# Performance work log

Hardware: AMD Instinct MI355X
Metric: run time of the kernel (lower is better)

Reference implementation:

```python
import jax, jax.numpy as jnp
import numpy as np

V_CNT = 10000
B = 16
N = B * V_CNT          # total nodes
K = 6                  # Chebyshev order
CH = [3, 128, 64, 32, 128]
G = 8                  # GroupNorm groups (divides 128, 64, 32)
EPS = 1e-5
AVG_DEG = 16


def setup_inputs() -> dict:
    key = jax.random.key(0)
    ks = jax.random.split(key, 8)
    n_edges = N * AVG_DEG
    inp = {
        "x": jax.random.normal(ks[0], (N, CH[0]), jnp.float32),
        "edge_index": jax.random.randint(ks[1], (2, n_edges), 0, N, jnp.int32).astype(jnp.int64),
    }
    for l in range(3):
        cin, cout = CH[l], CH[l + 1]
        s = (1.0 / (cin * K)) ** 0.5
        inp[f"W{l}"] = jax.random.uniform(ks[2 + l], (K, cin, cout), jnp.float32, -s, s)
        inp[f"b{l}"] = jnp.zeros((cout,), jnp.float32)
        inp[f"gamma{l}"] = jnp.ones((cout,), jnp.float32)
        inp[f"beta{l}"] = jnp.zeros((cout,), jnp.float32)
    din = V_CNT * CH[3]
    s = (1.0 / din) ** 0.5
    inp["W_last"] = jax.random.uniform(ks[5], (din, CH[4]), jnp.float32, -s, s)
    inp["b_last"] = jnp.zeros((CH[4],), jnp.float32)
    return inp


def _cheb_edge_weights(edge_index):
    # PyG ChebConv sym normalization with lambda_max=2: L_hat = L - I = -D^{-1/2} A D^{-1/2}
    row, col = edge_index[0], edge_index[1]
    deg = jax.ops.segment_sum(jnp.ones(row.shape, jnp.float32), row, num_segments=N)
    dis = jnp.where(deg > 0, jax.lax.rsqrt(jnp.maximum(deg, 1.0)), 0.0)  # deg^{-1/2}, inf->0
    return -dis[row] * dis[col], row, col


def _cheb_conv(x, row, col, w, W, b):
    # Chebyshev recursion: Tx0=x, Tx1=L_hat x, Tx_k = 2 L_hat Tx_{k-1} - Tx_{k-2}
    prop = lambda h: jax.ops.segment_sum(w[:, None] * h[col], row, num_segments=N)
    Tx0 = x
    out = Tx0 @ W[0]
    Tx1 = prop(Tx0)
    out = out + Tx1 @ W[1]
    for k in range(2, W.shape[0]):
        Tx2 = 2.0 * prop(Tx1) - Tx0
        out = out + Tx2 @ W[k]
        Tx0, Tx1 = Tx1, Tx2
    return out + b


def _group_norm(h, gamma, beta):
    n, C = h.shape
    hg = h.reshape(n, G, C // G)
    mu = hg.mean(axis=2, keepdims=True)
    var = hg.var(axis=2, keepdims=True)
    hg = (hg - mu) * jax.lax.rsqrt(var + EPS)
    return hg.reshape(n, C) * gamma + beta


def reference(x, edge_index, W0, b0, gamma0, beta0, W1, b1, gamma1, beta1,
              W2, b2, gamma2, beta2, W_last, b_last):
    w, row, col = _cheb_edge_weights(edge_index)
    Ws = [W0, W1, W2]
    bs = [b0, b1, b2]
    gs = [gamma0, gamma1, gamma2]
    betas = [beta0, beta1, beta2]
    h = x
    for l in range(3):
        h = _cheb_conv(h, row, col, w, Ws[l], bs[l])
        h = _group_norm(h, gs[l], betas[l])
        h = jax.nn.relu(h)
    h = h.reshape(-1, V_CNT * CH[3])  # [B, v_cnt*32]
    return h @ W_last + b_last
```

## Files before the change

### kernel.cpp

```cpp
#include <hip/hip_runtime.h>
#include <hip/hip_fp16.h>


#define NN 160000
#define EE 2560000
#define FD2 256
#define NBKT 625
#define BCAPL 13
#define ABLK 500
#define EPT 20

typedef __attribute__((ext_vector_type(8))) _Float16 half8;
typedef __attribute__((ext_vector_type(4))) float floatx4;

__device__ inline float2 h2f2(unsigned u) {
  __half2 h = __builtin_bit_cast(__half2, u);
  return __half22float2(h);
}
__device__ inline unsigned short f2h(float f) {
  return __builtin_bit_cast(unsigned short, __float2half_rn(f));
}
__device__ inline unsigned packh2(float a, float b) {
  return __builtin_bit_cast(unsigned, __floats2half2_rn(a, b));
}

template <int CIN, int COUT>
__device__ inline void combine_item(const float* __restrict__ W, unsigned short* __restrict__ Bt, int idx) {
  int co = idx % COUT;
  int j  = (idx / COUT) % 6;
  int ci = idx / (6 * COUT);
  float c0, c1, c2, c3, c4, c5;
  switch (j) {
    case 0:  c0 = 1;  c1 = 0;  c2 = -1; c3 = 0;   c4 = 1;  c5 = 0;   break;
    case 1:  c0 = 0;  c1 = 1;  c2 = 0;  c3 = -3;  c4 = 0;  c5 = 5;   break;
    case 2:  c0 = 0;  c1 = 0;  c2 = 2;  c3 = 0;   c4 = -8; c5 = 0;   break;
    case 3:  c0 = 0;  c1 = 0;  c2 = 0;  c3 = 4;   c4 = 0;  c5 = -20; break;
    case 4:  c0 = 0;  c1 = 0;  c2 = 0;  c3 = 0;   c4 = 8;  c5 = 0;   break;
    default: c0 = 0;  c1 = 0;  c2 = 0;  c3 = 0;   c4 = 0;  c5 = 16;  break;
  }
  float s = 0.f;
  s += c0 * W[(0 * CIN + ci) * COUT + co];
  s += c1 * W[(1 * CIN + ci) * COUT + co];
  s += c2 * W[(2 * CIN + ci) * COUT + co];
  s += c3 * W[(3 * CIN + ci) * COUT + co];
  s += c4 * W[(4 * CIN + ci) * COUT + co];
  s += c5 * W[(5 * CIN + ci) * COUT + co];
  Bt[(j * COUT + co) * CIN + ci] = f2h(s);
}

__global__ __launch_bounds__(256) void k_prep(const float* __restrict__ W0, const float* __restrict__ W1,
                                              const float* __restrict__ W2, const float* __restrict__ x,
                                              int* __restrict__ bcur, unsigned short* __restrict__ Cwt0,
                                              unsigned short* __restrict__ Cwt1, unsigned short* __restrict__ Cwt2,
                                              float* __restrict__ A3, unsigned short* __restrict__ TxAll) {
  int idx = blockIdx.x * 256 + threadIdx.x;
  if (idx < NBKT) { bcur[idx] = idx << BCAPL; return; }
  idx -= NBKT;
  if (idx < 128 * 32) {
    int co = idx >> 5, t = idx & 31;
    Cwt0[co * 32 + t] = (t < 18) ? f2h(W0[t * 128 + co]) : (unsigned short)0;
    return;
  }
  idx -= 128 * 32;
  if (idx < 128 * 6 * 64) { combine_item<128, 64>(W1, Cwt1, idx); return; }
  idx -= 128 * 6 * 64;
  if (idx < 64 * 6 * 32) { combine_item<64, 32>(W2, Cwt2, idx); return; }
  idx -= 64 * 6 * 32;
  if (idx < NN) {
    int i = idx;
    float v0 = x[i * 3], v1 = x[i * 3 + 1], v2 = x[i * 3 + 2];
    A3[i * 3] = v0; A3[i * 3 + 1] = v1; A3[i * 3 + 2] = v2;
    uint4* dst = reinterpret_cast<uint4*>(TxAll + (size_t)i * 32);
    uint4 z = make_uint4(0u, 0u, 0u, 0u);
    dst[0] = make_uint4(packh2(v0, v1), (unsigned)f2h(v2), 0u, 0u);
    dst[1] = z; dst[2] = z; dst[3] = z;
  }
}

__global__ __launch_bounds__(256) void k_bucketA(const int* __restrict__ ei,
                                                 int* __restrict__ bcur, unsigned* __restrict__ stg) {
  __shared__ int bcnt[NBKT];
  __shared__ int gbase[NBKT];
  int tid = threadIdx.x;
  for (int i = tid; i < NBKT; i += 256) bcnt[i] = 0;
  __syncthreads();
  int r[EPT];
  int e0 = blockIdx.x * (256 * EPT);
#pragma unroll
  for (int k = 0; k < EPT; k++) {
    int e = e0 + k * 256 + tid;
    r[k] = ei[e];
    atomicAdd(&bcnt[r[k] >> 8], 1);
  }
  __syncthreads();
  for (int i = tid; i < NBKT; i += 256) {
    gbase[i] = atomicAdd(&bcur[i], bcnt[i]);
    bcnt[i] = 0;
  }
  __syncthreads();
#pragma unroll
  for (int k = 0; k < EPT; k++) {
    int e = e0 + k * 256 + tid;
    int c = ei[EE + e];
    int b = r[k] >> 8;
    int off = atomicAdd(&bcnt[b], 1);
    int pos = gbase[b] + off;
    if (pos < ((b + 1) << BCAPL))
      stg[pos] = ((unsigned)(r[k] & 255) << 18) | (unsigned)c;
  }
}

__global__ __launch_bounds__(256) void k_bucketB1(const unsigned* __restrict__ stg, const int* __restrict__ bcur,
                                                  int* __restrict__ rowStart, float* __restrict__ dis,
                                                  int* __restrict__ deg) {
  __shared__ int degl[256];
  __shared__ int s[256];
  __shared__ int red[256];
  int b = blockIdx.x;
  int tid = threadIdx.x;
  int part = 0;
  for (int j = tid; j < NBKT; j += 256) {
    int cj = bcur[j] - (j << BCAPL);
    if (cj > (1 << BCAPL)) cj = 1 << BCAPL;
    if (j < b) part += cj;
  }
  red[tid] = part;
  degl[tid] = 0;
  __syncthreads();
  for (int off = 128; off > 0; off >>= 1) {
    if (tid < off) red[tid] += red[tid + off];
    __syncthreads();
  }
  int bbase = red[0];
  int cnt = bcur[b] - (b << BCAPL);
  if (cnt > (1 << BCAPL)) cnt = 1 << BCAPL;
  int base = b << BCAPL;
  for (int k = tid; k < cnt; k += 256)
    atomicAdd(&degl[stg[base + k] >> 18], 1);
  __syncthreads();
  int d = degl[tid];
  s[tid] = d;
  __syncthreads();
  for (int off = 1; off < 256; off <<= 1) {
    int t = (tid >= off) ? s[tid - off] : 0;
    __syncthreads();
    s[tid] += t;
    __syncthreads();
  }
  int r0 = b << 8;
  rowStart[r0 + tid] = bbase + s[tid] - d;
  dis[r0 + tid] = d > 0 ? rsqrtf((float)d) : 0.f;
  deg[r0 + tid] = d;
  if (b == 0 && tid == 0) rowStart[NN] = EE;
}

__global__ __launch_bounds__(256) void k_bucketB2(const unsigned* __restrict__ stg, const int* __restrict__ bcur,
                                                  const int* __restrict__ rowStart, const int* __restrict__ deg,
                                                  unsigned* __restrict__ ewc) {
  __shared__ int curs[256];
  int b = blockIdx.x;
  int tid = threadIdx.x;
  int r0 = b << 8;
  curs[tid] = rowStart[r0 + tid];
  __syncthreads();
  int cnt = bcur[b] - (b << BCAPL);
  if (cnt > (1 << BCAPL)) cnt = 1 << BCAPL;
  int base = b << BCAPL;
  for (int k = tid; k < cnt; k += 256) {
    unsigned u = stg[base + k];
    int rlow = u >> 18;
    int c = u & 0x3FFFFu;
    int pos = atomicAdd(&curs[rlow], 1);
    int dc = deg[c];
    if (dc > 8191) dc = 8191;
    ewc[pos] = (unsigned)c | ((unsigned)dc << 18);
  }
}

template <int MODE>
__global__ __launch_bounds__(256) void k_prop3(const float* __restrict__ Tsrc, float* __restrict__ Tdst,
                                               unsigned short* __restrict__ TxAll, int ks,
                                               const int* __restrict__ rowStart, const unsigned* __restrict__ ewc,
                                               const float* __restrict__ dis) {
  int i = blockIdx.x * 256 + threadIdx.x;
  if (i >= NN) return;
  float s0 = 0.f, s1 = 0.f, s2 = 0.f;
  int e = rowStart[i], e1 = rowStart[i + 1];
  for (; e + 3 < e1; e += 4) {
    unsigned u0 = ewc[e], u1 = ewc[e + 1], u2 = ewc[e + 2], u3 = ewc[e + 3];
    int c0 = u0 & 0x3FFFFu, c1 = u1 & 0x3FFFFu, c2 = u2 & 0x3FFFFu, c3 = u3 & 0x3FFFFu;
    unsigned d0 = u0 >> 18, d1 = u1 >> 18, d2 = u2 >> 18, d3 = u3 >> 18;
    float w0 = d0 ? rsqrtf((float)d0) : 0.f;
    float w1 = d1 ? rsqrtf((float)d1) : 0.f;
    float w2 = d2 ? rsqrtf((float)d2) : 0.f;
    float w3 = d3 ? rsqrtf((float)d3) : 0.f;
    s0 += w0 * Tsrc[c0 * 3] + w1 * Tsrc[c1 * 3] + w2 * Tsrc[c2 * 3] + w3 * Tsrc[c3 * 3];
    s1 += w0 * Tsrc[c0 * 3 + 1] + w1 * Tsrc[c1 * 3 + 1] + w2 * Tsrc[c2 * 3 + 1] + w3 * Tsrc[c3 * 3 + 1];
    s2 += w0 * Tsrc[c0 * 3 + 2] + w1 * Tsrc[c1 * 3 + 2] + w2 * Tsrc[c2 * 3 + 2] + w3 * Tsrc[c3 * 3 + 2];
  }
  for (; e < e1; e++) {
    unsigned u0 = ewc[e];
    int c0 = u0 & 0x3FFFFu;
    unsigned d0 = u0 >> 18;
    float w0 = d0 ? rsqrtf((float)d0) : 0.f;
    s0 += w0 * Tsrc[c0 * 3];
    s1 += w0 * Tsrc[c0 * 3 + 1];
    s2 += w0 * Tsrc[c0 * 3 + 2];
  }
  float ndr = -dis[i];
  float a0 = ndr * s0, a1 = ndr * s1, a2 = ndr * s2;
  if (MODE == 2) {
    a0 = 2.f * a0 - Tdst[i * 3];
    a1 = 2.f * a1 - Tdst[i * 3 + 1];
    a2 = 2.f * a2 - Tdst[i * 3 + 2];
  }
  Tdst[i * 3] = a0; Tdst[i * 3 + 1] = a1; Tdst[i * 3 + 2] = a2;
  unsigned short* tp = TxAll + i * 32 + ks * 3;
  tp[0] = f2h(a0); tp[1] = f2h(a1); tp[2] = f2h(a2);
}

__global__ __launch_bounds__(256) void k_gemm0gn(const unsigned short* __restrict__ A,
                                                 const unsigned short* __restrict__ Bt,
                                                 const float* __restrict__ bias, const float* __restrict__ gamma,
                                                 const float* __restrict__ beta, unsigned short* __restrict__ H) {
  constexpr int KP = 40;
  __shared__ unsigned short As[64 * KP];
  __shared__ unsigned short Bs[128 * KP];
  __shared__ float pb[128], pg[128], pe[128];
  int i0 = blockIdx.x * 64;
  for (int idx = threadIdx.x; idx < 64 * 4; idx += 256) {
    int row = idx >> 2, seg = idx & 3;
    uint4 v = ((const uint4*)A)[(size_t)(i0 + row) * 4 + seg];
    *reinterpret_cast<uint4*>(&As[row * KP + seg * 8]) = v;
  }
  for (int idx = threadIdx.x; idx < 128 * 4; idx += 256) {
    int row = idx >> 2, seg = idx & 3;
    uint4 v = ((const uint4*)Bt)[(size_t)row * 4 + seg];
    *reinterpret_cast<uint4*>(&Bs[row * KP + seg * 8]) = v;
  }
  if (threadIdx.x < 128) {
    pb[threadIdx.x] = bias[threadIdx.x];
    pg[threadIdx.x] = gamma[threadIdx.x];
    pe[threadIdx.x] = beta[threadIdx.x];
  }
  __syncthreads();
  int w = threadIdx.x >> 6, lane = threadIdx.x & 63;
  int mn = lane & 15, q = lane >> 4;
  floatx4 acc[8];
#pragma unroll
  for (int cb = 0; cb < 8; cb++) acc[cb] = {0.f, 0.f, 0.f, 0.f};
  half8 af = *reinterpret_cast<const half8*>(&As[(16 * w + mn) * KP + q * 8]);
#pragma unroll
  for (int cb = 0; cb < 8; cb++) {
    half8 bf = *reinterpret_cast<const half8*>(&Bs[(cb * 16 + mn) * KP + q * 8]);
    acc[cb] = __builtin_amdgcn_mfma_f32_16x16x32_f16(af, bf, acc[cb], 0, 0, 0);
  }
#pragma unroll
  for (int cb = 0; cb < 8; cb++) {
    int ch = cb * 16 + mn;
    float bs = pb[ch], ga = pg[ch], be = pe[ch];
    float v[4], S[4];
#pragma unroll
    for (int r = 0; r < 4; r++) { v[r] = acc[cb][r] + bs; S[r] = v[r]; }
#pragma unroll
    for (int m = 1; m < 16; m <<= 1)
#pragma unroll
      for (int r = 0; r < 4; r++) S[r] += __shfl_xor(S[r], m);
    float d[4], Q[4];
#pragma unroll
    for (int r = 0; r < 4; r++) { d[r] = v[r] - S[r] * 0.0625f; Q[r] = d[r] * d[r]; }
#pragma unroll
    for (int m = 1; m < 16; m <<= 1)
#pragma unroll
      for (int r = 0; r < 4; r++) Q[r] += __shfl_xor(Q[r], m);
#pragma unroll
    for (int r = 0; r < 4; r++) {
      float rs = rsqrtf(Q[r] * 0.0625f + 1e-5f);
      int i = i0 + 16 * w + q * 4 + r;
      H[(size_t)i * 128 + ch] = f2h(fmaxf(d[r] * rs * ga + be, 0.f));
    }
  }
}

template <int KDIM, int COUT>
__global__ __launch_bounds__(256) void k_gemm(const unsigned short* __restrict__ A,
                                              const unsigned short* __restrict__ Bt,
                                              unsigned short* __restrict__ Y) {
  constexpr int KP = KDIM + 8;
  __shared__ unsigned short As[64 * KP];
  __shared__ unsigned short Bs[64 * KP];
  int i0 = blockIdx.x * 64;
  int c0 = blockIdx.y * 64;
  for (int idx = threadIdx.x; idx < 64 * (KDIM / 8); idx += 256) {
    int row = idx / (KDIM / 8), seg = idx % (KDIM / 8);
    uint4 v = ((const uint4*)A)[(size_t)(i0 + row) * (KDIM / 8) + seg];
    *reinterpret_cast<uint4*>(&As[row * KP + seg * 8]) = v;
  }
  for (int idx = threadIdx.x; idx < 64 * (KDIM / 8); idx += 256) {
    int row = idx / (KDIM / 8), seg = idx % (KDIM / 8);
    uint4 v = ((const uint4*)Bt)[(size_t)(c0 + row) * (KDIM / 8) + seg];
    *reinterpret_cast<uint4*>(&Bs[row * KP + seg * 8]) = v;
  }
  __syncthreads();
  int w = threadIdx.x >> 6, lane = threadIdx.x & 63;
  int mn = lane & 15, q = lane >> 4;
  floatx4 acc[4];
#pragma unroll
  for (int cb = 0; cb < 4; cb++) acc[cb] = {0.f, 0.f, 0.f, 0.f};
#pragma unroll
  for (int ks = 0; ks < KDIM / 32; ks++) {
    half8 af = *reinterpret_cast<const half8*>(&As[(16 * w + mn) * KP + ks * 32 + q * 8]);
#pragma unroll
    for (int cb = 0; cb < 4; cb++) {
      half8 bf = *reinterpret_cast<const half8*>(&Bs[(cb * 16 + mn) * KP + ks * 32 + q * 8]);
      acc[cb] = __builtin_amdgcn_mfma_f32_16x16x32_f16(af, bf, acc[cb], 0, 0, 0);
    }
  }
#pragma unroll
  for (int cb = 0; cb < 4; cb++) {
    int jc = c0 + cb * 16 + mn;
    int slice = jc / COUT, cc = jc % COUT;
    unsigned short* dst = Y + (size_t)slice * NN * COUT + cc;
#pragma unroll
    for (int r = 0; r < 4; r++) {
      int i = i0 + 16 * w + q * 4 + r;
      dst[(size_t)i * COUT] = f2h(acc[cb][r]);
    }
  }
}

template <int CPN, int FUSE>
__global__ __launch_bounds__(256) void k_horner(const unsigned* __restrict__ Ysrc, unsigned* __restrict__ Ydst,
                                                const int* __restrict__ rowStart, const unsigned* __restrict__ ewc,
                                                const float* __restrict__ dis, unsigned* __restrict__ dst,
                                                const float* __restrict__ bias, const float* __restrict__ gamma,
                                                const float* __restrict__ beta) {
  int t = blockIdx.x * 256 + threadIdx.x;
  int i = t / CPN;
  int cp = t % CPN;
  float2 a = h2f2(Ydst[(size_t)i * CPN + cp]);
  float s0 = 0.f, s1 = 0.f;
  int e = rowStart[i], e1 = rowStart[i + 1];
  for (; e + 7 < e1; e += 8) {
    unsigned uu[8], u[8];
    float wv[8];
#pragma unroll
    for (int k = 0; k < 8; k++) uu[k] = ewc[e + k];
#pragma unroll
    for (int k = 0; k < 8; k++) u[k] = Ysrc[(size_t)(uu[k] & 0x3FFFFu) * CPN + cp];
#pragma unroll
    for (int k = 0; k < 8; k++) {
      unsigned dc = uu[k] >> 18;
      wv[k] = dc ? rsqrtf((float)dc) : 0.f;
    }
#pragma unroll
    for (int k = 0; k < 8; k++) {
      float2 f = h2f2(u[k]);
      s0 += wv[k] * f.x;
      s1 += wv[k] * f.y;
    }
  }
  for (; e < e1; e++) {
    unsigned u0 = ewc[e];
    unsigned dc = u0 >> 18;
    float w0 = dc ? rsqrtf((float)dc) : 0.f;
    float2 f0 = h2f2(Ysrc[(size_t)(u0 & 0x3FFFFu) * CPN + cp]);
    s0 += w0 * f0.x;
    s1 += w0 * f0.y;
  }
  float ndr = -dis[i];
  float v0 = a.x + ndr * s0, v1 = a.y + ndr * s1;
  if (FUSE == 0) {
    Ydst[(size_t)i * CPN + cp] = packh2(v0, v1);
  } else {
    constexpr int CPG = CPN / 4;
    constexpr int LPG = CPN / 8;
    v0 += bias[2 * cp];
    v1 += bias[2 * cp + 1];
    float s = v0 + v1;
#pragma unroll
    for (int m = 1; m < LPG; m <<= 1) s += __shfl_xor(s, m);
    float mean = s * (1.0f / CPG);
    float d0 = v0 - mean, d1 = v1 - mean;
    float qq = d0 * d0 + d1 * d1;
#pragma unroll
    for (int m = 1; m < LPG; m <<= 1) qq += __shfl_xor(qq, m);
    float rs = rsqrtf(qq * (1.0f / CPG) + 1e-5f);
    float o0 = fmaxf(d0 * rs * gamma[2 * cp] + beta[2 * cp], 0.f);
    float o1 = fmaxf(d1 * rs * gamma[2 * cp + 1] + beta[2 * cp + 1], 0.f);
    dst[(size_t)i * CPN + cp] = packh2(o0, o1);
  }
}

__global__ __launch_bounds__(256) void k_final1(const unsigned short* __restrict__ h3,
                                                const float* __restrict__ Wl,
                                                float* __restrict__ part) {
  __shared__ float hs[16 * FD2];
  __shared__ float red[2048];
  int d0 = blockIdx.x * FD2;
  const unsigned* h3u = reinterpret_cast<const unsigned*>(h3);
  for (int idx = threadIdx.x; idx < 16 * (FD2 / 2); idx += 256) {
    int b = idx / (FD2 / 2), dq = idx % (FD2 / 2);
    float2 f = h2f2(h3u[(size_t)b * 160000 + (d0 >> 1) + dq]);
    hs[b * FD2 + 2 * dq] = f.x;
    hs[b * FD2 + 2 * dq + 1] = f.y;
  }
  __syncthreads();
  int w = threadIdx.x >> 6, lane = threadIdx.x & 63;
  float a0[16], a1[16];
#pragma unroll
  for (int b = 0; b < 16; b++) { a0[b] = 0.f; a1[b] = 0.f; }
  const float* wp = Wl + (size_t)(d0 + w * (FD2 / 4)) * 128 + 2 * lane;
#pragma unroll 2
  for (int r = 0; r < FD2 / 4; r++) {
    float2 wv = *reinterpret_cast<const float2*>(wp + (size_t)r * 128);
    int row = w * (FD2 / 4) + r;
#pragma unroll
    for (int b = 0; b < 16; b++) {
      float h = hs[b * FD2 + row];
      a0[b] += wv.x * h;
      a1[b] += wv.y * h;
    }
  }
  float2* red2 = reinterpret_cast<float2*>(red);
  for (int ww = 0; ww < 4; ww++) {
    if (w == ww) {
#pragma unroll
      for (int b = 0; b < 16; b++) {
        if (ww == 0) {
          red2[b * 64 + lane] = make_float2(a0[b], a1[b]);
        } else {
          float2 r2 = red2[b * 64 + lane];
          r2.x += a0[b]; r2.y += a1[b];
          red2[b * 64 + lane] = r2;
        }
      }
    }
    __syncthreads();
  }
  for (int i = threadIdx.x; i < 2048; i += 256)
    part[(size_t)blockIdx.x * 2048 + i] = red[i];
}

__global__ __launch_bounds__(256) void k_final2(const float* __restrict__ part, const float* __restrict__ bl,
                                                float* __restrict__ out) {
  int o = blockIdx.x * 256 + threadIdx.x;
  float s = bl[o & 127];
#pragma unroll 10
  for (int p = 0; p < 1250; p++) s += part[(size_t)p * 2048 + o];
  out[o] = s;
}

extern "C" void kernel_launch(void* const* d_in, const int* in_sizes, int n_in,
                              void* d_out, int out_size, void* d_ws, size_t ws_size,
                              hipStream_t stream) {
  const float* x   = (const float*)d_in[0];
  const int*   ei  = (const int*)d_in[1];
  const float* W0  = (const float*)d_in[2];
  const float* b0  = (const float*)d_in[3];
  const float* g0  = (const float*)d_in[4];
  const float* be0 = (const float*)d_in[5];
  const float* W1  = (const float*)d_in[6];
  const float* b1  = (const float*)d_in[7];
  const float* g1  = (const float*)d_in[8];
  const float* be1 = (const float*)d_in[9];
  const float* W2  = (const float*)d_in[10];
  const float* b2  = (const float*)d_in[11];
  const float* g2  = (const float*)d_in[12];
  const float* be2 = (const float*)d_in[13];
  const float* Wl  = (const float*)d_in[14];
  const float* bl  = (const float*)d_in[15];
  float* out = (float*)d_out;
  (void)in_sizes; (void)n_in; (void)out_size; (void)ws_size;

  char* pw = (char*)d_ws;
  auto carve = [&](size_t bytes) -> void* {
    void* r = (void*)pw;
    pw += (bytes + 255) & ~(size_t)255;
    return r;
  };
  int*            bcur     = (int*)   carve((size_t)NBKT * 4);
  int*            rowStart = (int*)   carve((size_t)(NN + 1) * 4);
  float*          dis      = (float*) carve((size_t)NN * 4);
  int*            deg      = (int*)   carve((size_t)NN * 4);
  unsigned*       ewc      = (unsigned*)carve((size_t)EE * 4);
  unsigned short* Cwt0     = (unsigned short*)carve((size_t)128 * 32 * 2);
  unsigned short* Cwt1     = (unsigned short*)carve((size_t)384 * 128 * 2);
  unsigned short* Cwt2     = (unsigned short*)carve((size_t)192 * 64 * 2);
  unsigned short* TxAll    = (unsigned short*)carve((size_t)NN * 32 * 2);
  float*          A3       = (float*) carve((size_t)NN * 3 * 4);
  float*          B3       = (float*) carve((size_t)NN * 3 * 4);
  unsigned short* Hbuf     = (unsigned short*)carve((size_t)NN * 128 * 2);
  unsigned short* Ybuf     = (unsigned short*)carve((size_t)NN * 384 * 2);
  float*          part     = (float*) carve((size_t)1250 * 2048 * 4);
  unsigned*       stg      = (unsigned*)Ybuf;

  k_prep<<<884, 256, 0, stream>>>(W0, W1, W2, x, bcur, Cwt0, Cwt1, Cwt2, A3, TxAll);
  k_bucketA<<<ABLK, 256, 0, stream>>>(ei, bcur, stg);
  k_bucketB1<<<NBKT, 256, 0, stream>>>(stg, bcur, rowStart, dis, deg);
  k_bucketB2<<<NBKT, 256, 0, stream>>>(stg, bcur, rowStart, deg, ewc);

  k_prop3<1><<<625, 256, 0, stream>>>(A3, B3, TxAll, 1, rowStart, ewc, dis);
  k_prop3<2><<<625, 256, 0, stream>>>(B3, A3, TxAll, 2, rowStart, ewc, dis);
  k_prop3<2><<<625, 256, 0, stream>>>(A3, B3, TxAll, 3, rowStart, ewc, dis);
  k_prop3<2><<<625, 256, 0, stream>>>(B3, A3, TxAll, 4, rowStart, ewc, dis);
  k_prop3<2><<<625, 256, 0, stream>>>(A3, B3, TxAll, 5, rowStart, ewc, dis);
  k_gemm0gn<<<2500, 256, 0, stream>>>(TxAll, Cwt0, b0, g0, be0, Hbuf);

  k_gemm<128, 64><<<dim3(2500, 6), 256, 0, stream>>>(Hbuf, Cwt1, Ybuf);
  for (int j = 4; j >= 1; j--)
    k_horner<32, 0><<<20000, 256, 0, stream>>>((unsigned*)(Ybuf + (size_t)(j + 1) * NN * 64),
                                               (unsigned*)(Ybuf + (size_t)j * NN * 64), rowStart, ewc, dis,
                                               nullptr, nullptr, nullptr, nullptr);
  k_horner<32, 1><<<20000, 256, 0, stream>>>((unsigned*)(Ybuf + (size_t)NN * 64),
                                             (unsigned*)Ybuf, rowStart, ewc, dis,
                                             (unsigned*)Hbuf, b1, g1, be1);

  k_gemm<64, 32><<<dim3(2500, 3), 256, 0, stream>>>(Hbuf, Cwt2, Ybuf);
  for (int j = 4; j >= 1; j--)
    k_horner<16, 0><<<10000, 256, 0, stream>>>((unsigned*)(Ybuf + (size_t)(j + 1) * NN * 32),
                                               (unsigned*)(Ybuf + (size_t)j * NN * 32), rowStart, ewc, dis,
                                               nullptr, nullptr, nullptr, nullptr);
  k_horner<16, 1><<<10000, 256, 0, stream>>>((unsigned*)(Ybuf + (size_t)NN * 32),
                                             (unsigned*)Ybuf, rowStart, ewc, dis,
                                             (unsigned*)Hbuf, b2, g2, be2);

  k_final1<<<1250, 256, 0, stream>>>(Hbuf, Wl, part);
  k_final2<<<8, 256, 0, stream>>>(part, bl, out);
}
```

Baseline: 1.223 ms.

## Fuse CSR build, propagation and Horner passes into cooperative grid-synced kernels

Several chains of small dependent kernel launches are replaced with cooperative kernels that use grid.sync(). These cover the bucket sort and CSR build, the five 3-channel propagation steps, and the Horner passes for layers 1 and 2. The aim is to remove per-launch overhead and tail gaps between short kernels. In exchange the Horner passes run on a fixed grid of 1024 blocks with grid-stride loops, which may lower memory-level parallelism. Co-residency also constrains occupancy: 625 blocks must fit at once for the CSR and propagation kernels.

```diff
diff --git a/kernel.cpp b/kernel.cpp
--- a/kernel.cpp
+++ b/kernel.cpp
@@ -1,5 +1,8 @@
 #include <hip/hip_runtime.h>
 #include <hip/hip_fp16.h>
+#include <hip/hip_cooperative_groups.h>
+
+namespace cg = cooperative_groups;
 
 
 #define NN 160000
@@ -7,8 +10,7 @@
 #define FD2 256
 #define NBKT 625
 #define BCAPL 13
-#define ABLK 500
-#define EPT 20
+#define EPTC 16
 
 typedef __attribute__((ext_vector_type(8))) _Float16 half8;
 typedef __attribute__((ext_vector_type(4))) float floatx4;
@@ -50,12 +52,10 @@
 
 __global__ __launch_bounds__(256) void k_prep(const float* __restrict__ W0, const float* __restrict__ W1,
                                               const float* __restrict__ W2, const float* __restrict__ x,
-                                              int* __restrict__ bcur, unsigned short* __restrict__ Cwt0,
+                                              unsigned short* __restrict__ Cwt0,
                                               unsigned short* __restrict__ Cwt1, unsigned short* __restrict__ Cwt2,
                                               float* __restrict__ A3, unsigned short* __restrict__ TxAll) {
   int idx = blockIdx.x * 256 + threadIdx.x;
-  if (idx < NBKT) { bcur[idx] = idx << BCAPL; return; }
-  idx -= NBKT;
   if (idx < 128 * 32) {
     int co = idx >> 5, t = idx & 31;
     Cwt0[co * 32 + t] = (t < 18) ? f2h(W0[t * 128 + co]) : (unsigned short)0;
@@ -77,47 +77,47 @@
   }
 }
 
-__global__ __launch_bounds__(256) void k_bucketA(const int* __restrict__ ei,
-                                                 int* __restrict__ bcur, unsigned* __restrict__ stg) {
+__global__ __launch_bounds__(256, 3) void k_csr(const int* __restrict__ ei, int* __restrict__ bcur,
+                                                unsigned* __restrict__ stg, int* __restrict__ rowStart,
+                                                float* __restrict__ dis, int* __restrict__ deg,
+                                                unsigned* __restrict__ ewc) {
+  cg::grid_group grid = cg::this_grid();
   __shared__ int bcnt[NBKT];
   __shared__ int gbase[NBKT];
+  __shared__ int degl[256];
+  __shared__ int sscan[256];
+  __shared__ int red[256];
+  __shared__ int curs[256];
   int tid = threadIdx.x;
+  int b = blockIdx.x;
   for (int i = tid; i < NBKT; i += 256) bcnt[i] = 0;
-  __syncthreads();
-  int r[EPT];
-  int e0 = blockIdx.x * (256 * EPT);
-#pragma unroll
-  for (int k = 0; k < EPT; k++) {
+  if (tid == 0) bcur[b] = b << BCAPL;
+  __syncthreads();
+  int r[EPTC];
+  int e0 = b * (256 * EPTC);
+#pragma unroll
+  for (int k = 0; k < EPTC; k++) {
     int e = e0 + k * 256 + tid;
     r[k] = ei[e];
     atomicAdd(&bcnt[r[k] >> 8], 1);
   }
-  __syncthreads();
+  grid.sync();
   for (int i = tid; i < NBKT; i += 256) {
     gbase[i] = atomicAdd(&bcur[i], bcnt[i]);
     bcnt[i] = 0;
   }
   __syncthreads();
 #pragma unroll
-  for (int k = 0; k < EPT; k++) {
+  for (int k = 0; k < EPTC; k++) {
     int e = e0 + k * 256 + tid;
     int c = ei[EE + e];
-    int b = r[k] >> 8;
-    int off = atomicAdd(&bcnt[b], 1);
-    int pos = gbase[b] + off;
-    if (pos < ((b + 1) << BCAPL))
+    int bb = r[k] >> 8;
+    int off = atomicAdd(&bcnt[bb], 1);
+    int pos = gbase[bb] + off;
+    if (pos < ((bb + 1) << BCAPL))
       stg[pos] = ((unsigned)(r[k] & 255) << 18) | (unsigned)c;
   }
-}
-
-__global__ __launch_bounds__(256) void k_bucketB1(const unsigned* __restrict__ stg, const int* __restrict__ bcur,
-                                                  int* __restrict__ rowStart, float* __restrict__ dis,
-                                                  int* __restrict__ deg) {
-  __shared__ int degl[256];
-  __shared__ int s[256];
-  __shared__ int red[256];
-  int b = blockIdx.x;
-  int tid = threadIdx.x;
+  grid.sync();
   int part = 0;
   for (int j = tid; j < NBKT; j += 256) {
     int cj = bcur[j] - (j << BCAPL);
@@ -139,33 +139,22 @@
     atomicAdd(&degl[stg[base + k] >> 18], 1);
   __syncthreads();
   int d = degl[tid];
-  s[tid] = d;
+  sscan[tid] = d;
   __syncthreads();
   for (int off = 1; off < 256; off <<= 1) {
-    int t = (tid >= off) ? s[tid - off] : 0;
+    int t = (tid >= off) ? sscan[tid - off] : 0;
     __syncthreads();
-    s[tid] += t;
+    sscan[tid] += t;
     __syncthreads();
   }
   int r0 = b << 8;
-  rowStart[r0 + tid] = bbase + s[tid] - d;
+  int rsv = bbase + sscan[tid] - d;
+  rowStart[r0 + tid] = rsv;
   dis[r0 + tid] = d > 0 ? rsqrtf((float)d) : 0.f;
   deg[r0 + tid] = d;
   if (b == 0 && tid == 0) rowStart[NN] = EE;
-}
-
-__global__ __launch_bounds__(256) void k_bucketB2(const unsigned* __restrict__ stg, const int* __restrict__ bcur,
-                                                  const int* __restrict__ rowStart, const int* __restrict__ deg,
-                                                  unsigned* __restrict__ ewc) {
-  __shared__ int curs[256];
-  int b = blockIdx.x;
-  int tid = threadIdx.x;
-  int r0 = b << 8;
-  curs[tid] = rowStart[r0 + tid];
-  __syncthreads();
-  int cnt = bcur[b] - (b << BCAPL);
-  if (cnt > (1 << BCAPL)) cnt = 1 << BCAPL;
-  int base = b << BCAPL;
+  curs[tid] = rsv;
+  grid.sync();
   for (int k = tid; k < cnt; k += 256) {
     unsigned u = stg[base + k];
     int rlow = u >> 18;
@@ -178,12 +167,10 @@
 }
 
 template <int MODE>
-__global__ __launch_bounds__(256) void k_prop3(const float* __restrict__ Tsrc, float* __restrict__ Tdst,
-                                               unsigned short* __restrict__ TxAll, int ks,
-                                               const int* __restrict__ rowStart, const unsigned* __restrict__ ewc,
-                                               const float* __restrict__ dis) {
-  int i = blockIdx.x * 256 + threadIdx.x;
-  if (i >= NN) return;
+__device__ void prop_step(const float* __restrict__ Tsrc, float* __restrict__ Tdst,
+                          unsigned short* __restrict__ TxAll, int ks,
+                          const int* __restrict__ rowStart, const unsigned* __restrict__ ewc,
+                          const float* __restrict__ dis, int i) {
   float s0 = 0.f, s1 = 0.f, s2 = 0.f;
   int e = rowStart[i], e1 = rowStart[i + 1];
   for (; e + 3 < e1; e += 4) {
@@ -219,6 +206,20 @@
   tp[0] = f2h(a0); tp[1] = f2h(a1); tp[2] = f2h(a2);
 }
 
+__global__ __launch_bounds__(256, 3) void k_prop3coop(float* __restrict__ A3, float* __restrict__ B3,
+                                                      unsigned short* __restrict__ TxAll,
+                                                      const int* __restrict__ rowStart,
+                                                      const unsigned* __restrict__ ewc,
+                                                      const float* __restrict__ dis) {
+  cg::grid_group grid = cg::this_grid();
+  int i = blockIdx.x * 256 + threadIdx.x;
+  prop_step<1>(A3, B3, TxAll, 1, rowStart, ewc, dis, i); grid.sync();
+  prop_step<2>(B3, A3, TxAll, 2, rowStart, ewc, dis, i); grid.sync();
+  prop_step<2>(A3, B3, TxAll, 3, rowStart, ewc, dis, i); grid.sync();
+  prop_step<2>(B3, A3, TxAll, 4, rowStart, ewc, dis, i); grid.sync();
+  prop_step<2>(A3, B3, TxAll, 5, rowStart, ewc, dis, i);
+}
+
 __global__ __launch_bounds__(256) void k_gemm0gn(const unsigned short* __restrict__ A,
                                                  const unsigned short* __restrict__ Bt,
                                                  const float* __restrict__ bias, const float* __restrict__ gamma,
@@ -261,23 +262,23 @@
     float bs = pb[ch], ga = pg[ch], be = pe[ch];
     float v[4], S[4];
 #pragma unroll
-    for (int r = 0; r < 4; r++) { v[r] = acc[cb][r] + bs; S[r] = v[r]; }
+    for (int rr = 0; rr < 4; rr++) { v[rr] = acc[cb][rr] + bs; S[rr] = v[rr]; }
 #pragma unroll
     for (int m = 1; m < 16; m <<= 1)
 #pragma unroll
-      for (int r = 0; r < 4; r++) S[r] += __shfl_xor(S[r], m);
-    float d[4], Q[4];
-#pragma unroll
-    for (int r = 0; r < 4; r++) { d[r] = v[r] - S[r] * 0.0625f; Q[r] = d[r] * d[r]; }
+      for (int rr = 0; rr < 4; rr++) S[rr] += __shfl_xor(S[rr], m);
+    float dd[4], Q[4];
+#pragma unroll
+    for (int rr = 0; rr < 4; rr++) { dd[rr] = v[rr] - S[rr] * 0.0625f; Q[rr] = dd[rr] * dd[rr]; }
 #pragma unroll
     for (int m = 1; m < 16; m <<= 1)
 #pragma unroll
-      for (int r = 0; r < 4; r++) Q[r] += __shfl_xor(Q[r], m);
-#pragma unroll
-    for (int r = 0; r < 4; r++) {
-      float rs = rsqrtf(Q[r] * 0.0625f + 1e-5f);
-      int i = i0 + 16 * w + q * 4 + r;
-      H[(size_t)i * 128 + ch] = f2h(fmaxf(d[r] * rs * ga + be, 0.f));
+      for (int rr = 0; rr < 4; rr++) Q[rr] += __shfl_xor(Q[rr], m);
+#pragma unroll
+    for (int rr = 0; rr < 4; rr++) {
+      float rs = rsqrtf(Q[rr] * 0.0625f + 1e-5f);
+      int i = i0 + 16 * w + q * 4 + rr;
+      H[(size_t)i * 128 + ch] = f2h(fmaxf(dd[rr] * rs * ga + be, 0.f));
     }
   }
 }
@@ -322,74 +323,95 @@
     int slice = jc / COUT, cc = jc % COUT;
     unsigned short* dst = Y + (size_t)slice * NN * COUT + cc;
 #pragma unroll
-    for (int r = 0; r < 4; r++) {
-      int i = i0 + 16 * w + q * 4 + r;
-      dst[(size_t)i * COUT] = f2h(acc[cb][r]);
+    for (int rr = 0; rr < 4; rr++) {
+      int i = i0 + 16 * w + q * 4 + rr;
+      dst[(size_t)i * COUT] = f2h(acc[cb][rr]);
     }
   }
 }
 
 template <int CPN, int FUSE>
-__global__ __launch_bounds__(256) void k_horner(const unsigned* __restrict__ Ysrc, unsigned* __restrict__ Ydst,
-                                                const int* __restrict__ rowStart, const unsigned* __restrict__ ewc,
-                                                const float* __restrict__ dis, unsigned* __restrict__ dst,
-                                                const float* __restrict__ bias, const float* __restrict__ gamma,
-                                                const float* __restrict__ beta) {
-  int t = blockIdx.x * 256 + threadIdx.x;
-  int i = t / CPN;
-  int cp = t % CPN;
-  float2 a = h2f2(Ydst[(size_t)i * CPN + cp]);
-  float s0 = 0.f, s1 = 0.f;
-  int e = rowStart[i], e1 = rowStart[i + 1];
-  for (; e + 7 < e1; e += 8) {
-    unsigned uu[8], u[8];
-    float wv[8];
-#pragma unroll
-    for (int k = 0; k < 8; k++) uu[k] = ewc[e + k];
-#pragma unroll
-    for (int k = 0; k < 8; k++) u[k] = Ysrc[(size_t)(uu[k] & 0x3FFFFu) * CPN + cp];
-#pragma unroll
-    for (int k = 0; k < 8; k++) {
-      unsigned dc = uu[k] >> 18;
-      wv[k] = dc ? rsqrtf((float)dc) : 0.f;
-    }
-#pragma unroll
-    for (int k = 0; k < 8; k++) {
-      float2 f = h2f2(u[k]);
-      s0 += wv[k] * f.x;
-      s1 += wv[k] * f.y;
-    }
-  }
-  for (; e < e1; e++) {
-    unsigned u0 = ewc[e];
-    unsigned dc = u0 >> 18;
-    float w0 = dc ? rsqrtf((float)dc) : 0.f;
-    float2 f0 = h2f2(Ysrc[(size_t)(u0 & 0x3FFFFu) * CPN + cp]);
-    s0 += w0 * f0.x;
-    s1 += w0 * f0.y;
-  }
-  float ndr = -dis[i];
-  float v0 = a.x + ndr * s0, v1 = a.y + ndr * s1;
-  if (FUSE == 0) {
-    Ydst[(size_t)i * CPN + cp] = packh2(v0, v1);
-  } else {
-    constexpr int CPG = CPN / 4;
-    constexpr int LPG = CPN / 8;
-    v0 += bias[2 * cp];
-    v1 += bias[2 * cp + 1];
-    float s = v0 + v1;
-#pragma unroll
-    for (int m = 1; m < LPG; m <<= 1) s += __shfl_xor(s, m);
-    float mean = s * (1.0f / CPG);
-    float d0 = v0 - mean, d1 = v1 - mean;
-    float qq = d0 * d0 + d1 * d1;
-#pragma unroll
-    for (int m = 1; m < LPG; m <<= 1) qq += __shfl_xor(qq, m);
-    float rs = rsqrtf(qq * (1.0f / CPG) + 1e-5f);
-    float o0 = fmaxf(d0 * rs * gamma[2 * cp] + beta[2 * cp], 0.f);
-    float o1 = fmaxf(d1 * rs * gamma[2 * cp + 1] + beta[2 * cp + 1], 0.f);
-    dst[(size_t)i * CPN + cp] = packh2(o0, o1);
-  }
+__device__ void horner_pass(const unsigned* __restrict__ Ysrc, unsigned* __restrict__ Ydst,
+                            const int* __restrict__ rowStart, const unsigned* __restrict__ ewc,
+                            const float* __restrict__ dis, unsigned* __restrict__ dst,
+                            const float* __restrict__ bias, const float* __restrict__ gamma,
+                            const float* __restrict__ beta, int gid, int gsize) {
+  for (int t = gid; t < NN * CPN; t += gsize) {
+    int i = t / CPN;
+    int cp = t % CPN;
+    float2 a = h2f2(Ydst[(size_t)i * CPN + cp]);
+    float s0 = 0.f, s1 = 0.f;
+    int e = rowStart[i], e1 = rowStart[i + 1];
+    for (; e + 7 < e1; e += 8) {
+      unsigned uu[8], u[8];
+      float wv[8];
+#pragma unroll
+      for (int k = 0; k < 8; k++) uu[k] = ewc[e + k];
+#pragma unroll
+      for (int k = 0; k < 8; k++) u[k] = Ysrc[(size_t)(uu[k] & 0x3FFFFu) * CPN + cp];
+#pragma unroll
+      for (int k = 0; k < 8; k++) {
+        unsigned dc = uu[k] >> 18;
+        wv[k] = dc ? rsqrtf((float)dc) : 0.f;
+      }
+#pragma unroll
+      for (int k = 0; k < 8; k++) {
+        float2 f = h2f2(u[k]);
+        s0 += wv[k] * f.x;
+        s1 += wv[k] * f.y;
+      }
+    }
+    for (; e < e1; e++) {
+      unsigned u0 = ewc[e];
+      unsigned dc = u0 >> 18;
+      float w0 = dc ? rsqrtf((float)dc) : 0.f;
+      float2 f0 = h2f2(Ysrc[(size_t)(u0 & 0x3FFFFu) * CPN + cp]);
+      s0 += w0 * f0.x;
+      s1 += w0 * f0.y;
+    }
+    float ndr = -dis[i];
+    float v0 = a.x + ndr * s0, v1 = a.y + ndr * s1;
+    if (FUSE == 0) {
+      Ydst[(size_t)i * CPN + cp] = packh2(v0, v1);
+    } else {
+      constexpr int CPG = CPN / 4;
+      constexpr int LPG = CPN / 8;
+      v0 += bias[2 * cp];
+      v1 += bias[2 * cp + 1];
+      float s = v0 + v1;
+#pragma unroll
+      for (int m = 1; m < LPG; m <<= 1) s += __shfl_xor(s, m);
+      float mean = s * (1.0f / CPG);
+      float d0 = v0 - mean, d1 = v1 - mean;
+      float qq = d0 * d0 + d1 * d1;
+#pragma unroll
+      for (int m = 1; m < LPG; m <<= 1) qq += __shfl_xor(qq, m);
+      float rs = rsqrtf(qq * (1.0f / CPG) + 1e-5f);
+      float o0 = fmaxf(d0 * rs * gamma[2 * cp] + beta[2 * cp], 0.f);
+      float o1 = fmaxf(d1 * rs * gamma[2 * cp + 1] + beta[2 * cp + 1], 0.f);
+      dst[(size_t)i * CPN + cp] = packh2(o0, o1);
+    }
+  }
+}
+
+template <int CPN>
+__global__ __launch_bounds__(256, 4) void k_hcoop(unsigned* __restrict__ Y,
+                                                  const int* __restrict__ rowStart,
+                                                  const unsigned* __restrict__ ewc,
+                                                  const float* __restrict__ dis,
+                                                  unsigned* __restrict__ dst,
+                                                  const float* __restrict__ bias,
+                                                  const float* __restrict__ gamma,
+                                                  const float* __restrict__ beta) {
+  cg::grid_group grid = cg::this_grid();
+  int gid = blockIdx.x * 256 + threadIdx.x;
+  int gsize = gridDim.x * 256;
+  for (int j = 4; j >= 1; j--) {
+    horner_pass<CPN, 0>(Y + (size_t)(j + 1) * NN * CPN, Y + (size_t)j * NN * CPN,
+                        rowStart, ewc, dis, nullptr, nullptr, nullptr, nullptr, gid, gsize);
+    grid.sync();
+  }
+  horner_pass<CPN, 1>(Y + (size_t)NN * CPN, Y, rowStart, ewc, dis, dst, bias, gamma, beta, gid, gsize);
 }
 
 __global__ __launch_bounds__(256) void k_final1(const unsigned short* __restrict__ h3,
@@ -495,35 +517,38 @@
   float*          part     = (float*) carve((size_t)1250 * 2048 * 4);
   unsigned*       stg      = (unsigned*)Ybuf;
 
-  k_prep<<<884, 256, 0, stream>>>(W0, W1, W2, x, bcur, Cwt0, Cwt1, Cwt2, A3, TxAll);
-  k_bucketA<<<ABLK, 256, 0, stream>>>(ei, bcur, stg);
-  k_bucketB1<<<NBKT, 256, 0, stream>>>(stg, bcur, rowStart, dis, deg);
-  k_bucketB2<<<NBKT, 256, 0, stream>>>(stg, bcur, rowStart, deg, ewc);
-
-  k_prop3<1><<<625, 256, 0, stream>>>(A3, B3, TxAll, 1, rowStart, ewc, dis);
-  k_prop3<2><<<625, 256, 0, stream>>>(B3, A3, TxAll, 2, rowStart, ewc, dis);
-  k_prop3<2><<<625, 256, 0, stream>>>(A3, B3, TxAll, 3, rowStart, ewc, dis);
-  k_prop3<2><<<625, 256, 0, stream>>>(B3, A3, TxAll, 4, rowStart, ewc, dis);
-  k_prop3<2><<<625, 256, 0, stream>>>(A3, B3, TxAll, 5, rowStart, ewc, dis);
+  k_prep<<<881, 256, 0, stream>>>(W0, W1, W2, x, Cwt0, Cwt1, Cwt2, A3, TxAll);
+
+  {
+    void* a[] = {(void*)&ei, (void*)&bcur, (void*)&stg, (void*)&rowStart,
+                 (void*)&dis, (void*)&deg, (void*)&ewc};
+    hipLaunchCooperativeKernel((const void*)&k_csr, dim3(NBKT), dim3(256), a, 0, stream);
+  }
+
+  {
+    void* a[] = {(void*)&A3, (void*)&B3, (void*)&TxAll, (void*)&rowStart,
+                 (void*)&ewc, (void*)&dis};
+    hipLaunchCooperativeKernel((const void*)&k_prop3coop, dim3(NBKT), dim3(256), a, 0, stream);
+  }
   k_gemm0gn<<<2500, 256, 0, stream>>>(TxAll, Cwt0, b0, g0, be0, Hbuf);
 
   k_gemm<128, 64><<<dim3(2500, 6), 256, 0, stream>>>(Hbuf, Cwt1, Ybuf);
-  for (int j = 4; j >= 1; j--)
-    k_horner<32, 0><<<20000, 256, 0, stream>>>((unsigned*)(Ybuf + (size_t)(j + 1) * NN * 64),
-                                               (unsigned*)(Ybuf + (size_t)j * NN * 64), rowStart, ewc, dis,
-                                               nullptr, nullptr, nullptr, nullptr);
-  k_horner<32, 1><<<20000, 256, 0, stream>>>((unsigned*)(Ybuf + (size_t)NN * 64),
-                                             (unsigned*)Ybuf, rowStart, ewc, dis,
-                                             (unsigned*)Hbuf, b1, g1, be1);
+  {
+    unsigned* Y1 = (unsigned*)Ybuf;
+    unsigned* H1 = (unsigned*)Hbuf;
+    void* a[] = {(void*)&Y1, (void*)&rowStart, (void*)&ewc, (void*)&dis,
+                 (void*)&H1, (void*)&b1, (void*)&g1, (void*)&be1};
+    hipLaunchCooperativeKernel((const void*)&k_hcoop<32>, dim3(1024), dim3(256), a, 0, stream);
+  }
 
   k_gemm<64, 32><<<dim3(2500, 3), 256, 0, stream>>>(Hbuf, Cwt2, Ybuf);
-  for (int j = 4; j >= 1; j--)
-    k_horner<16, 0><<<10000, 256, 0, stream>>>((unsigned*)(Ybuf + (size_t)(j + 1) * NN * 32),
-                                               (unsigned*)(Ybuf + (size_t)j * NN * 32), rowStart, ewc, dis,
-                                               nullptr, nullptr, nullptr, nullptr);
-  k_horner<16, 1><<<10000, 256, 0, stream>>>((unsigned*)(Ybuf + (size_t)NN * 32),
-                                             (unsigned*)Ybuf, rowStart, ewc, dis,
-                                             (unsigned*)Hbuf, b2, g2, be2);
+  {
+    unsigned* Y2 = (unsigned*)Ybuf;
+    unsigned* H2 = (unsigned*)Hbuf;
+    void* a[] = {(void*)&Y2, (void*)&rowStart, (void*)&ewc, (void*)&dis,
+                 (void*)&H2, (void*)&b2, (void*)&g2, (void*)&be2};
+    hipLaunchCooperativeKernel((const void*)&k_hcoop<16>, dim3(1024), dim3(256), a, 0, stream);
+  }
 
   k_final1<<<1250, 256, 0, stream>>>(Hbuf, Wl, part);
   k_final2<<<8, 256, 0, stream>>>(part, bl, out);
```

Measured after the change: 3.104 ms. +153.9%, slower.
